# Kernel tuning notes

Measured on AMD Instinct MI355X. Metric: run time of the kernel, lower is better.

Reference implementation:

```python
import jax, jax.numpy as jnp
import numpy as np

K_WRITE = 4
NUM_SLOTS = 16
VOCAB = 50257
D = 512


def layer_norm(x, g, b, eps=1e-5):
    mu = jnp.mean(x, axis=-1, keepdims=True)
    var = jnp.mean((x - mu) ** 2, axis=-1, keepdims=True)
    return (x - mu) * jax.lax.rsqrt(var + eps) * g + b


def setup_inputs() -> dict:
    key = jax.random.key(0)
    ks = jax.random.split(key, 16)
    B, T = 32, 2048
    s = lambda *sh: 1.0 / np.sqrt(sh[0])
    seq = jax.random.randint(ks[0], (B, T), 0, VOCAB)
    embed = jax.random.normal(ks[1], (VOCAB, D), jnp.float32) * 0.02
    W1 = jax.random.normal(ks[2], (D, 2 * D), jnp.float32) * s(D)
    b1 = jnp.zeros((2 * D,), jnp.float32)
    W2 = jax.random.normal(ks[3], (2 * D, D), jnp.float32) * s(2 * D)
    b2 = jnp.zeros((D,), jnp.float32)
    ln_g = jnp.ones((D,), jnp.float32)
    ln_b = jnp.zeros((D,), jnp.float32)
    Wg = jax.random.normal(ks[4], (D, NUM_SLOTS), jnp.float32) * s(D)
    bg = jnp.zeros((NUM_SLOTS,), jnp.float32)
    Wr = jax.random.normal(ks[5], (D, D), jnp.float32) * s(D)
    br = jnp.zeros((D,), jnp.float32)
    Wo = jax.random.normal(ks[6], (D, VOCAB), jnp.float32) * s(D)
    bo = jnp.zeros((VOCAB,), jnp.float32)
    return dict(seq=seq, embed=embed, W1=W1, b1=b1, W2=W2, b2=b2, ln_g=ln_g,
                ln_b=ln_b, Wg=Wg, bg=bg, Wr=Wr, br=br, Wo=Wo, bo=bo)


def forward(seq, embed, W1, b1, W2, b2, ln_g, ln_b, Wg, bg, Wr, br, Wo, bo):
    # Encoder: embed -> FFN residual -> layernorm
    h = embed[seq]                                  # [B,T,D]
    ff = jax.nn.relu(h @ W1 + b1) @ W2 + b2
    hiddens = layer_norm(h + ff, ln_g, ln_b)        # [B,T,D]

    ctx_h = hiddens[:, :-1, :]                      # [B,T-1,D]
    B, Tm1, Dd = ctx_h.shape
    k_w = min(K_WRITE, Tm1)

    # write_to_memory: gate -> topk -> gather -> scatter into zero memory
    gate_scores = jnp.mean(ctx_h @ Wg + bg, axis=-1)          # [B,T-1]
    _, top_idx = jax.lax.top_k(gate_scores, k_w)              # [B,k_w]
    gathered = jnp.take_along_axis(ctx_h, top_idx[:, :, None], axis=1)  # [B,k_w,D]
    slot_idx = jnp.arange(k_w) % NUM_SLOTS                    # unique since k_w<=slots
    mem = jnp.zeros((B, NUM_SLOTS, Dd), ctx_h.dtype).at[:, slot_idx, :].set(gathered)

    # small attention read
    q = hiddens[:, -1, :] @ Wr + br                 # [B,D]
    scores = jnp.einsum('bsd,bd->bs', mem, q)       # [B,slots]
    attn = jax.nn.softmax(scores, axis=-1)
    ctx = jnp.einsum('bs,bsd->bd', attn, mem)       # [B,D]
    return ctx @ Wo + bo                            # [B,vocab]


def reference(seq, embed, W1, b1, W2, b2, ln_g, ln_b, Wg, bg, Wr, br, Wo, bo):
    return forward(seq, embed, W1, b1, W2, b2, ln_g, ln_b, Wg, bg, Wr, br, Wo, bo)
```

## Files before the change

### kernel.cpp

```cpp
#include <hip/hip_runtime.h>
#include <stdint.h>

typedef __attribute__((ext_vector_type(8))) short bf16x8;
typedef __attribute__((ext_vector_type(4))) float f32x4;
typedef __attribute__((ext_vector_type(16))) float f32x16;
typedef unsigned short ushortT;

#define DEV static __device__ __forceinline__

DEV unsigned short f2bf(float x) {
  union { float f; unsigned u; } v; v.f = x;
  unsigned r = v.u + 0x7fffu + ((v.u >> 16) & 1u);
  return (unsigned short)(r >> 16);
}
DEV float bf2f(unsigned short b) {
  union { unsigned u; float f; } v; v.u = ((unsigned)b) << 16; return v.f;
}
DEV void gll16(const void* g, void* l) {
  __builtin_amdgcn_global_load_lds((const __attribute__((address_space(1))) void*)g,
                                   (__attribute__((address_space(3))) void*)l, 16, 0, 0);
}

#define VMW(n) asm volatile("s_waitcnt vmcnt(" #n ")" ::: "memory")
#define RAWBAR() __builtin_amdgcn_s_barrier()
#define SCHED0() __builtin_amdgcn_sched_barrier(0)

__global__ void kPrep(const float* __restrict__ W1, const float* __restrict__ W2,
                      const float* __restrict__ Wg, const float* __restrict__ ln_g,
                      ushortT* __restrict__ W1t, ushortT* __restrict__ W2t,
                      float* __restrict__ gw, float* __restrict__ wgm) {
  const size_t t = (size_t)blockIdx.x * 256 + threadIdx.x;
  if (t < 524288) {
    int n = (int)(t & 1023), k = (int)(t >> 10);
    W1t[(size_t)n * 512 + k] = f2bf(W1[(size_t)k * 1024 + n]);
  } else if (t < 1048576) {
    size_t u = t - 524288;
    int n = (int)(u & 511), k = (int)(u >> 9);
    W2t[(size_t)n * 1024 + k] = f2bf(W2[(size_t)k * 512 + n]);
  } else if (t < 1048576 + 512) {
    int c = (int)(t - 1048576);
    float s = 0.f;
    for (int j = 0; j < 16; ++j) s += Wg[c * 16 + j];
    float m = s * (1.0f / 16.0f);
    wgm[c] = m;
    gw[c] = ln_g[c] * m;
  }
}

__global__ void kPrep2(const float* __restrict__ gw, const float* __restrict__ wgm,
                       const float* __restrict__ ln_b, const float* __restrict__ bg,
                       float* __restrict__ consts) {
  const int tid = threadIdx.x;
  float a = gw[tid];
  float c = ln_b[tid] * wgm[tid];
  #pragma unroll
  for (int s = 1; s < 64; s <<= 1) { a += __shfl_xor(a, s); c += __shfl_xor(c, s); }
  __shared__ float red[8][2];
  const int wv = tid >> 6, ln = tid & 63;
  if (ln == 0) { red[wv][0] = a; red[wv][1] = c; }
  __syncthreads();
  if (tid == 0) {
    float Cg = 0, Cb0 = 0;
    for (int k = 0; k < 8; ++k) { Cg += red[k][0]; Cb0 += red[k][1]; }
    float bgm = 0;
    for (int j = 0; j < 16; ++j) bgm += bg[j];
    bgm *= (1.0f / 16.0f);
    consts[0] = Cg; consts[1] = Cb0 + bgm; consts[2] = bgm;
  }
}

__global__ void kEmbed(const int* __restrict__ seq, const float* __restrict__ embed,
                       ushortT* __restrict__ h) {
  const size_t t = (size_t)blockIdx.x * 256 + threadIdx.x;
  const size_t row = t >> 6;
  const int seg = (int)(t & 63) * 8;
  const int tok = seq[row];
  const float4* src = (const float4*)(embed + (size_t)tok * 512 + seg);
  float4 x = src[0], y = src[1];
  uint4 u;
  u.x = (unsigned)f2bf(x.x) | ((unsigned)f2bf(x.y) << 16);
  u.y = (unsigned)f2bf(x.z) | ((unsigned)f2bf(x.w) << 16);
  u.z = (unsigned)f2bf(y.x) | ((unsigned)f2bf(y.y) << 16);
  u.w = (unsigned)f2bf(y.z) | ((unsigned)f2bf(y.w) << 16);
  *(uint4*)(h + row * 512 + seg) = u;
}

__global__ __launch_bounds__(512, 2) void kG1p(const ushortT* __restrict__ h,
                                               const ushortT* __restrict__ W1t,
                                               const float* __restrict__ b1,
                                               ushortT* __restrict__ Y) {
  __shared__ __align__(16) ushortT SH[32768];
  const int tid = threadIdx.x, w = tid >> 6, l = tid & 63;
  const int b = blockIdx.x, xcd = b & 7, loc = b >> 3;
  const int nt = loc & 3, mtl = loc >> 2;
  const size_t m0 = (size_t)(xcd * 16 + mtl) * 256;
  const int n0 = nt * 256;
  const int rl = l & 15, gq = l >> 4;
  f32x4 acc[4][8] = {};

  auto stage = [&](int buf, int k0) {
    #pragma unroll
    for (int q = 0; q < 2; ++q) {
      const int c = w * 2 + q;
      gll16(h + (m0 + c * 16 + rl) * 512 + k0 + gq * 8, &SH[buf * 8192 + c * 512]);
      gll16(W1t + (size_t)(n0 + c * 16 + rl) * 512 + k0 + gq * 8, &SH[16384 + buf * 8192 + c * 512]);
    }
  };

  const int wr = w >> 1, wc = w & 1, l8 = l * 8;
  auto compute = [&](int buf) {
    bf16x8 a[4], bb[8];
    #pragma unroll
    for (int i = 0; i < 4; ++i)
      a[i] = *(const bf16x8*)&SH[buf * 8192 + (wr * 4 + i) * 512 + l8];
    #pragma unroll
    for (int j = 0; j < 8; ++j)
      bb[j] = *(const bf16x8*)&SH[16384 + buf * 8192 + (wc * 8 + j) * 512 + l8];
    #pragma unroll
    for (int i = 0; i < 4; ++i)
      #pragma unroll
      for (int j = 0; j < 8; ++j)
        acc[i][j] = __builtin_amdgcn_mfma_f32_16x16x32_bf16(a[i], bb[j], acc[i][j], 0, 0, 0);
  };

  stage(0, 0);
  VMW(0); RAWBAR();
  for (int t = 0; t < 16; ++t) {
    if (t < 15) stage((t + 1) & 1, (t + 1) * 32);
    SCHED0();
    compute(t & 1);
    SCHED0();
    VMW(0); RAWBAR();
  }

  float bv[8];
  #pragma unroll
  for (int j = 0; j < 8; ++j) bv[j] = b1[n0 + wc * 128 + j * 16 + rl];

  #pragma unroll
  for (int P = 0; P < 4; ++P) {
    __syncthreads();
    if (wr == P) {
      #pragma unroll
      for (int i = 0; i < 4; ++i) {
        #pragma unroll
        for (int j = 0; j < 8; ++j) {
          const int cl = wc * 128 + j * 16 + rl;
          #pragma unroll
          for (int r = 0; r < 4; ++r) {
            const int lr = i * 16 + gq * 4 + r;
            float v = acc[i][j][r] + bv[j];
            v = v > 0.0f ? v : 0.0f;
            SH[lr * 266 + cl] = f2bf(v);
          }
        }
      }
    }
    __syncthreads();
    #pragma unroll
    for (int it = 0; it < 4; ++it) {
      const int row = it * 16 + (tid >> 5);
      const int c8 = (tid & 31) * 8;
      uint4 v = *(const uint4*)&SH[row * 266 + c8];
      *(uint4*)&Y[(m0 + P * 64 + row) * 1024 + n0 + c8] = v;
    }
  }
}

__global__ __launch_bounds__(512, 2) void kG2p(const ushortT* __restrict__ Yb,
                                               const ushortT* __restrict__ W2t,
                                               const ushortT* __restrict__ h,
                                               const float* __restrict__ b2,
                                               const float* __restrict__ gw,
                                               float* __restrict__ partS, int R0) {
  __shared__ __align__(16) ushortT As[2][256 * 32];
  __shared__ __align__(16) ushortT Bs[2][128 * 32];
  __shared__ float part[256][2][3];
  const int tid = threadIdx.x, w = tid >> 6, l = tid & 63;
  const int b = blockIdx.x, xcd = b & 7, loc = b >> 3;
  const int nt = loc & 3, mtl = loc >> 2;
  const size_t m0 = (size_t)(xcd * 16 + mtl) * 256;
  const int n0 = nt * 128;
  const int rl = l & 15, gq = l >> 4;
  f32x4 acc[4][4] = {};

  auto stage = [&](int buf, int k0) {
    #pragma unroll
    for (int q = 0; q < 2; ++q) {
      const int c = w * 2 + q;
      gll16(Yb + (m0 + c * 16 + rl) * 1024 + k0 + gq * 8, &As[buf][c * 512]);
    }
    gll16(W2t + (size_t)(n0 + w * 16 + rl) * 1024 + k0 + gq * 8, &Bs[buf][w * 512]);
  };

  const int wr = w >> 1, wc = w & 1, l8 = l * 8;
  auto compute = [&](int buf) {
    bf16x8 a[4], bb[4];
    #pragma unroll
    for (int i = 0; i < 4; ++i)
      a[i] = *(const bf16x8*)&As[buf][(wr * 4 + i) * 512 + l8];
    #pragma unroll
    for (int j = 0; j < 4; ++j)
      bb[j] = *(const bf16x8*)&Bs[buf][(wc * 4 + j) * 512 + l8];
    #pragma unroll
    for (int i = 0; i < 4; ++i)
      #pragma unroll
      for (int j = 0; j < 4; ++j)
        acc[i][j] = __builtin_amdgcn_mfma_f32_16x16x32_bf16(a[i], bb[j], acc[i][j], 0, 0, 0);
  };

  stage(0, 0);
  VMW(0); RAWBAR();
  for (int t = 0; t < 32; ++t) {
    if (t < 31) stage((t + 1) & 1, (t + 1) * 32);
    SCHED0();
    compute(t & 1);
    SCHED0();
    VMW(0); RAWBAR();
  }

  #pragma unroll
  for (int i = 0; i < 4; ++i) {
    #pragma unroll
    for (int r = 0; r < 4; ++r) {
      const int rowl = wr * 64 + i * 16 + gq * 4 + r;
      const size_t grow = (size_t)R0 + m0 + rowl;
      float s1 = 0, s2 = 0, s3 = 0;
      #pragma unroll
      for (int j = 0; j < 4; ++j) {
        const int col = n0 + wc * 64 + j * 16 + rl;
        const float z = acc[i][j][r] + b2[col] + bf2f(h[grow * 512 + col]);
        s1 += z; s2 += z * z; s3 += z * gw[col];
      }
      #pragma unroll
      for (int s = 1; s < 16; s <<= 1) {
        s1 += __shfl_xor(s1, s);
        s2 += __shfl_xor(s2, s);
        s3 += __shfl_xor(s3, s);
      }
      if (rl == 0) { part[rowl][wc][0] = s1; part[rowl][wc][1] = s2; part[rowl][wc][2] = s3; }
    }
  }
  __syncthreads();
  if (tid < 256) {
    const size_t grow = (size_t)R0 + m0 + tid;
    const float S1 = part[tid][0][0] + part[tid][1][0];
    const float S2 = part[tid][0][1] + part[tid][1][1];
    const float S3 = part[tid][0][2] + part[tid][1][2];
    float* p = partS + grow * 16 + nt * 4;
    p[0] = S1; p[1] = S2; p[2] = S3;
  }
}

__global__ void kTop(const float* __restrict__ partS, const float* __restrict__ consts,
                     float* __restrict__ scores, int* __restrict__ cidx,
                     int* __restrict__ ccnt) {
  const int b = blockIdx.x, tid = threadIdx.x;
  const float Cg = consts[0], Cb = consts[1];
  float v0 = -1e30f, v1 = -1e30f, v2 = -1e30f, v3 = -1e30f;
  for (int i = tid; i < 2047; i += 256) {
    const size_t row = (size_t)b * 2048 + i;
    const float* p = partS + row * 16;
    const float S1 = p[0] + p[4] + p[8] + p[12];
    const float S2 = p[1] + p[5] + p[9] + p[13];
    const float S3 = p[2] + p[6] + p[10] + p[14];
    const float mu = S1 * (1.0f / 512.0f);
    const float var = S2 * (1.0f / 512.0f) - mu * mu;
    const float x = rsqrtf(var + 1e-5f) * (S3 - mu * Cg) + Cb;
    scores[row] = x;
    if (x > v3) {
      if (x > v0)      { v3 = v2; v2 = v1; v1 = v0; v0 = x; }
      else if (x > v1) { v3 = v2; v2 = v1; v1 = x; }
      else if (x > v2) { v3 = v2; v2 = x; }
      else             { v3 = x; }
    }
  }
  __shared__ float lv[256][4];
  lv[tid][0] = v0; lv[tid][1] = v1; lv[tid][2] = v2; lv[tid][3] = v3;
  __syncthreads();
  for (int s = 128; s > 0; s >>= 1) {
    if (tid < s) {
      float m[8] = { lv[tid][0], lv[tid][1], lv[tid][2], lv[tid][3],
                     lv[tid + s][0], lv[tid + s][1], lv[tid + s][2], lv[tid + s][3] };
      #pragma unroll
      for (int k = 0; k < 4; ++k) {
        int mx = k;
        #pragma unroll
        for (int j2 = k + 1; j2 < 8; ++j2) if (m[j2] > m[mx]) mx = j2;
        const float tv = m[k]; m[k] = m[mx]; m[mx] = tv;
        lv[tid][k] = m[k];
      }
    }
    __syncthreads();
  }
  __shared__ int cnt;
  __shared__ float thr;
  if (tid == 0) { thr = lv[0][3] - 0.03f; cnt = 0; }
  __syncthreads();
  const float th = thr;
  const float* sc = scores + (size_t)b * 2048;
  for (int i = tid; i < 2047; i += 256) {
    if (sc[i] >= th) {
      const int p = atomicAdd(&cnt, 1);
      if (p < 24) cidx[b * 24 + p] = i;
    }
  }
  __syncthreads();
  if (tid == 0) ccnt[b] = cnt < 24 ? cnt : 24;
}

__global__ void kCompact(const int* __restrict__ ccnt, const int* __restrict__ cidx,
                         int* __restrict__ offs, int* __restrict__ rowsb,
                         int* __restrict__ rowsl, int* __restrict__ plast,
                         int* __restrict__ nrp) {
  const int tid = threadIdx.x;
  if (tid >= 32) return;
  int off = 0, nc = 0;
  for (int k = 0; k < 32; ++k) { const int c = ccnt[k]; if (k < tid) off += c; nc += c; }
  offs[tid] = off;
  const int cnt = ccnt[tid];
  for (int j = 0; j < cnt; ++j) { rowsb[off + j] = tid; rowsl[off + j] = cidx[tid * 24 + j]; }
  rowsb[nc + tid] = tid; rowsl[nc + tid] = 2047; plast[tid] = nc + tid;
  if (tid == 0) { offs[32] = nc; nrp[0] = nc + 32; }
}

__global__ void kGather(const int* __restrict__ nrp, const int* __restrict__ rowsb,
                        const int* __restrict__ rowsl, const int* __restrict__ seq,
                        const float* __restrict__ embed, float* __restrict__ H2) {
  const int p = blockIdx.x;
  if (p >= nrp[0]) return;
  const int b = rowsb[p], lr = rowsl[p];
  const size_t gr = (size_t)b * 2048 + lr;
  const int tok = seq[gr];
  const float* src = embed + (size_t)tok * 512;
  float* dst = H2 + (size_t)p * 512;
  for (int c = threadIdx.x; c < 512; c += 128) dst[c] = src[c];
}

__global__ __launch_bounds__(256) void kR1(const int* __restrict__ nrp,
                                           const float* __restrict__ H2,
                                           const float* __restrict__ W1,
                                           const float* __restrict__ b1,
                                           float* __restrict__ Y2) {
  const int p = blockIdx.y;
  if (p >= nrp[0]) return;
  const int col = blockIdx.x * 256 + threadIdx.x;
  __shared__ float hrow[512];
  for (int c = threadIdx.x; c < 512; c += 256) hrow[c] = H2[(size_t)p * 512 + c];
  __syncthreads();
  float a0 = 0, a1 = 0, a2 = 0, a3 = 0;
  #pragma unroll 4
  for (int k = 0; k < 512; k += 4) {
    a0 = fmaf(hrow[k + 0], W1[(size_t)(k + 0) * 1024 + col], a0);
    a1 = fmaf(hrow[k + 1], W1[(size_t)(k + 1) * 1024 + col], a1);
    a2 = fmaf(hrow[k + 2], W1[(size_t)(k + 2) * 1024 + col], a2);
    a3 = fmaf(hrow[k + 3], W1[(size_t)(k + 3) * 1024 + col], a3);
  }
  const float v = a0 + a1 + a2 + a3 + b1[col];
  Y2[(size_t)p * 1024 + col] = v > 0.0f ? v : 0.0f;
}

__global__ __launch_bounds__(256) void kR2(const int* __restrict__ nrp,
                                           const float* __restrict__ Y2,
                                           const float* __restrict__ W2,
                                           const float* __restrict__ b2,
                                           float* __restrict__ F2) {
  const int p = blockIdx.y;
  if (p >= nrp[0]) return;
  const int col = blockIdx.x * 256 + threadIdx.x;
  __shared__ float yrow[1024];
  for (int c = threadIdx.x; c < 1024; c += 256) yrow[c] = Y2[(size_t)p * 1024 + c];
  __syncthreads();
  float a0 = 0, a1 = 0, a2 = 0, a3 = 0;
  #pragma unroll 4
  for (int k = 0; k < 1024; k += 4) {
    a0 = fmaf(yrow[k + 0], W2[(size_t)(k + 0) * 512 + col], a0);
    a1 = fmaf(yrow[k + 1], W2[(size_t)(k + 1) * 512 + col], a1);
    a2 = fmaf(yrow[k + 2], W2[(size_t)(k + 2) * 512 + col], a2);
    a3 = fmaf(yrow[k + 3], W2[(size_t)(k + 3) * 512 + col], a3);
  }
  F2[(size_t)p * 512 + col] = a0 + a1 + a2 + a3 + b2[col];
}

__global__ void kR3(const int* __restrict__ nrp, const float* __restrict__ H2,
                    const float* __restrict__ F2, const float* __restrict__ ln_g,
                    const float* __restrict__ ln_b, const float* __restrict__ wgm,
                    const float* __restrict__ consts, float* __restrict__ LNR,
                    float* __restrict__ cscore) {
  const int p = blockIdx.x;
  if (p >= nrp[0]) return;
  const int tid = threadIdx.x;
  const int c0 = tid, c1 = tid + 256;
  const float z0 = H2[(size_t)p * 512 + c0] + F2[(size_t)p * 512 + c0];
  const float z1 = H2[(size_t)p * 512 + c1] + F2[(size_t)p * 512 + c1];
  float s1 = z0 + z1, s2 = z0 * z0 + z1 * z1;
  #pragma unroll
  for (int s = 1; s < 64; s <<= 1) { s1 += __shfl_xor(s1, s); s2 += __shfl_xor(s2, s); }
  __shared__ float red[4][2];
  __shared__ float stats[2];
  const int wv = tid >> 6, ln = tid & 63;
  if (ln == 0) { red[wv][0] = s1; red[wv][1] = s2; }
  __syncthreads();
  if (tid == 0) {
    const float S1 = red[0][0] + red[1][0] + red[2][0] + red[3][0];
    const float S2 = red[0][1] + red[1][1] + red[2][1] + red[3][1];
    const float mu = S1 * (1.0f / 512.0f);
    const float var = S2 * (1.0f / 512.0f) - mu * mu;
    stats[0] = mu; stats[1] = rsqrtf(var + 1e-5f);
  }
  __syncthreads();
  const float mu = stats[0], rstd = stats[1];
  const float l0 = (z0 - mu) * rstd * ln_g[c0] + ln_b[c0];
  const float l1 = (z1 - mu) * rstd * ln_g[c1] + ln_b[c1];
  LNR[(size_t)p * 512 + c0] = l0;
  LNR[(size_t)p * 512 + c1] = l1;
  float sp = l0 * wgm[c0] + l1 * wgm[c1];
  #pragma unroll
  for (int s = 1; s < 64; s <<= 1) sp += __shfl_xor(sp, s);
  if (ln == 0) red[wv][0] = sp;
  __syncthreads();
  if (tid == 0) cscore[p] = red[0][0] + red[1][0] + red[2][0] + red[3][0] + consts[2];
}

__global__ void kSel(const int* __restrict__ ccnt, const int* __restrict__ offs,
                     const int* __restrict__ rowsl, const int* __restrict__ plast,
                     const float* __restrict__ cscore, const float* __restrict__ LNR,
                     const float* __restrict__ Wr, const float* __restrict__ br,
                     float* __restrict__ ctx, ushortT* __restrict__ ctxB) {
  const int b = blockIdx.x, tid = threadIdx.x;
  __shared__ int psel[4];
  __shared__ float lnl[512];
  __shared__ float qs[512];
  __shared__ float aw[4];
  __shared__ float red[4][4];
  if (tid == 0) {
    const int cnt = ccnt[b], off = offs[b];
    float scv[24]; int lr[24]; bool tk[24];
    for (int j = 0; j < cnt; ++j) { scv[j] = cscore[off + j]; lr[j] = rowsl[off + j]; tk[j] = false; }
    for (int k = 0; k < 4; ++k) {
      int best = -1;
      for (int j = 0; j < cnt; ++j) {
        if (tk[j]) continue;
        if (best < 0 || scv[j] > scv[best] || (scv[j] == scv[best] && lr[j] < lr[best])) best = j;
      }
      tk[best] = true;
      psel[k] = off + best;
    }
  }
  __syncthreads();
  const int pl = plast[b];
  for (int c = tid; c < 512; c += 256) lnl[c] = LNR[(size_t)pl * 512 + c];
  __syncthreads();
  #pragma unroll
  for (int cc = 0; cc < 2; ++cc) {
    const int col = tid + cc * 256;
    float s = br[col];
    for (int d = 0; d < 512; ++d) s = fmaf(lnl[d], Wr[(size_t)d * 512 + col], s);
    qs[col] = s;
  }
  __syncthreads();
  const int p0 = psel[0], p1 = psel[1], p2 = psel[2], p3 = psel[3];
  float ps[4] = {0, 0, 0, 0};
  for (int d = tid; d < 512; d += 256) {
    const float qv = qs[d];
    ps[0] = fmaf(qv, LNR[(size_t)p0 * 512 + d], ps[0]);
    ps[1] = fmaf(qv, LNR[(size_t)p1 * 512 + d], ps[1]);
    ps[2] = fmaf(qv, LNR[(size_t)p2 * 512 + d], ps[2]);
    ps[3] = fmaf(qv, LNR[(size_t)p3 * 512 + d], ps[3]);
  }
  #pragma unroll
  for (int s = 1; s < 64; s <<= 1) {
    ps[0] += __shfl_xor(ps[0], s); ps[1] += __shfl_xor(ps[1], s);
    ps[2] += __shfl_xor(ps[2], s); ps[3] += __shfl_xor(ps[3], s);
  }
  const int wv = tid >> 6, ln = tid & 63;
  if (ln == 0) { red[wv][0] = ps[0]; red[wv][1] = ps[1]; red[wv][2] = ps[2]; red[wv][3] = ps[3]; }
  __syncthreads();
  if (tid == 0) {
    const float s0 = red[0][0] + red[1][0] + red[2][0] + red[3][0];
    const float s1 = red[0][1] + red[1][1] + red[2][1] + red[3][1];
    const float s2 = red[0][2] + red[1][2] + red[2][2] + red[3][2];
    const float s3 = red[0][3] + red[1][3] + red[2][3] + red[3][3];
    const float m = fmaxf(fmaxf(fmaxf(s0, s1), fmaxf(s2, s3)), 0.0f);
    const float e0 = expf(s0 - m), e1 = expf(s1 - m), e2 = expf(s2 - m), e3 = expf(s3 - m);
    const float den = e0 + e1 + e2 + e3 + 12.0f * expf(-m);
    aw[0] = e0 / den; aw[1] = e1 / den; aw[2] = e2 / den; aw[3] = e3 / den;
  }
  __syncthreads();
  const float a0 = aw[0], a1 = aw[1], a2 = aw[2], a3 = aw[3];
  #pragma unroll
  for (int cc = 0; cc < 2; ++cc) {
    const int col = tid + cc * 256;
    const float v = a0 * LNR[(size_t)p0 * 512 + col] + a1 * LNR[(size_t)p1 * 512 + col]
                  + a2 * LNR[(size_t)p2 * 512 + col] + a3 * LNR[(size_t)p3 * 512 + col];
    ctx[(size_t)b * 512 + col] = v;
    ctxB[(size_t)b * 512 + col] = f2bf(v);
  }
}

__global__ __launch_bounds__(512) void kOutM(const ushortT* __restrict__ ctxB,
                                             const float* __restrict__ Wo,
                                             float* __restrict__ partial) {
  const int tid = threadIdx.x, w = tid >> 6, l = tid & 63;
  const int ky = blockIdx.y;
  int col = blockIdx.x * 256 + w * 32 + (l & 31);
  const bool cv = col < 50257;
  if (!cv) col = 50256;
  const int kg = (l >> 5) * 8;
  const int kb = ky * 256;
  bf16x8 afr[16];
  #pragma unroll
  for (int ks = 0; ks < 16; ++ks)
    afr[ks] = *(const bf16x8*)&ctxB[(size_t)(l & 31) * 512 + kb + ks * 16 + kg];
  f32x16 acc = {};
  #pragma unroll
  for (int ks = 0; ks < 16; ++ks) {
    const float* wp = Wo + (size_t)(kb + ks * 16 + kg) * 50257 + col;
    float wv[8];
    #pragma unroll
    for (int j = 0; j < 8; ++j) wv[j] = wp[(size_t)j * 50257];
    bf16x8 bfr;
    #pragma unroll
    for (int j = 0; j < 8; ++j) bfr[j] = (short)f2bf(wv[j]);
    acc = __builtin_amdgcn_mfma_f32_32x32x16_bf16(afr[ks], bfr, acc, 0, 0, 0);
  }
  if (cv) {
    #pragma unroll
    for (int r = 0; r < 16; ++r) {
      const int row = (r & 3) + 8 * (r >> 2) + 4 * (l >> 5);
      partial[((size_t)ky * 32 + row) * 50257 + col] = acc[r];
    }
  }
}

__global__ __launch_bounds__(256) void kOutRed(const float* __restrict__ partial,
                                               const float* __restrict__ bo,
                                               float* __restrict__ out) {
  const size_t i = (size_t)blockIdx.x * 256 + threadIdx.x;
  if (i >= (size_t)32 * 50257) return;
  const int col = (int)(i % 50257);
  float s = bo[col];
  #pragma unroll
  for (int q = 0; q < 2; ++q) s += partial[(size_t)q * 32 * 50257 + i];
  out[i] = s;
}

extern "C" void kernel_launch(void* const* d_in, const int* in_sizes, int n_in,
                              void* d_out, int out_size, void* d_ws, size_t ws_size,
                              hipStream_t stream) {
  const int*   seq   = (const int*)  d_in[0];
  const float* embed = (const float*)d_in[1];
  const float* W1    = (const float*)d_in[2];
  const float* b1    = (const float*)d_in[3];
  const float* W2    = (const float*)d_in[4];
  const float* b2    = (const float*)d_in[5];
  const float* ln_g  = (const float*)d_in[6];
  const float* ln_b  = (const float*)d_in[7];
  const float* Wg    = (const float*)d_in[8];
  const float* bg    = (const float*)d_in[9];
  const float* Wr    = (const float*)d_in[10];
  const float* br    = (const float*)d_in[11];
  const float* Wo    = (const float*)d_in[12];
  const float* bo    = (const float*)d_in[13];
  float* out = (float*)d_out;
  char* ws = (char*)d_ws;

  ushortT* W1t   = (ushortT*)(ws + 0);
  ushortT* W2t   = (ushortT*)(ws + 1048576);
  float* gw      = (float*)(ws + 2097152);
  float* wgm     = (float*)(ws + 2099200);
  float* consts  = (float*)(ws + 2101248);
  ushortT* h     = (ushortT*)(ws + 2101504);
  ushortT* Ybuf  = (ushortT*)(ws + 69210368);
  float* partial = (float*)(ws + 69210368);
  float* scores  = (float*)(ws + 136319232);
  int* cidx      = (int*)(ws + 136581376);
  int* ccnt      = (int*)(ws + 136584448);
  int* offs      = (int*)(ws + 136584576);
  int* nrp       = (int*)(ws + 136584832);
  int* plast     = (int*)(ws + 136585088);
  int* rowsb     = (int*)(ws + 136585344);
  int* rowsl     = (int*)(ws + 136588672);
  float* partS   = (float*)(ws + 136592000);
  float* H2      = (float*)(ws + 136592000);
  float* Y2      = (float*)(ws + 138295936);
  float* F2      = (float*)(ws + 141703808);
  float* LNR     = (float*)(ws + 143407744);
  float* csc     = (float*)(ws + 145111680);
  float* ctxb    = (float*)(ws + 145115008);
  ushortT* ctxB  = (ushortT*)(ws + 145180544);

  kPrep <<<4098, 256, 0, stream>>>(W1, W2, Wg, ln_g, W1t, W2t, gw, wgm);
  kPrep2<<<1, 512, 0, stream>>>(gw, wgm, ln_b, bg, consts);
  kEmbed<<<16384, 256, 0, stream>>>(seq, embed, h);
  for (int c = 0; c < 2; ++c) {
    kG1p<<<512, 512, 0, stream>>>(h + (size_t)c * 32768 * 512, W1t, b1, Ybuf);
    kG2p<<<512, 512, 0, stream>>>(Ybuf, W2t, h, b2, gw, partS, c * 32768);
  }
  kTop    <<<32, 256, 0, stream>>>(partS, consts, scores, cidx, ccnt);
  kCompact<<<1, 64, 0, stream>>>(ccnt, cidx, offs, rowsb, rowsl, plast, nrp);
  kGather <<<800, 128, 0, stream>>>(nrp, rowsb, rowsl, seq, embed, H2);
  kR1<<<dim3(4, 800), 256, 0, stream>>>(nrp, H2, W1, b1, Y2);
  kR2<<<dim3(2, 800), 256, 0, stream>>>(nrp, Y2, W2, b2, F2);
  kR3<<<800, 256, 0, stream>>>(nrp, H2, F2, ln_g, ln_b, wgm, consts, LNR, csc);
  kSel<<<32, 256, 0, stream>>>(ccnt, offs, rowsl, plast, csc, LNR, Wr, br, ctxb, ctxB);
  kOutM<<<dim3(197, 2), 512, 0, stream>>>(ctxB, Wo, partial);
  kOutRed<<<(32 * 50257 + 255) / 256, 256, 0, stream>>>(partial, bo, out);
}
```

Baseline: 447.7 us.

## Double K-tile depth in FFN GEMMs and raise wave priority around MFMA

Both FFN GEMM kernels now stage 64-wide K tiles per iteration (as two 32-wide halves) instead of 32-wide ones. This halves the number of main-loop iterations and barriers. The wait on the next prefetch moves to before compute using a partial vmcnt, and MFMA bursts are bracketed with s_setprio to favour waves issuing matrix math. The trade-off is a larger LDS footprint (128 KB in the first GEMM, about 100 KB in the second), which likely limits each CU to one block despite launch bounds requesting two, reducing latency hiding across blocks.

```diff
diff --git a/kernel.cpp b/kernel.cpp
--- a/kernel.cpp
+++ b/kernel.cpp
@@ -24,6 +24,8 @@
 #define VMW(n) asm volatile("s_waitcnt vmcnt(" #n ")" ::: "memory")
 #define RAWBAR() __builtin_amdgcn_s_barrier()
 #define SCHED0() __builtin_amdgcn_sched_barrier(0)
+#define PRIO1() __builtin_amdgcn_s_setprio(1)
+#define PRIO0() __builtin_amdgcn_s_setprio(0)
 
 __global__ void kPrep(const float* __restrict__ W1, const float* __restrict__ W2,
                       const float* __restrict__ Wg, const float* __restrict__ ln_g,
@@ -89,7 +91,7 @@
                                                const ushortT* __restrict__ W1t,
                                                const float* __restrict__ b1,
                                                ushortT* __restrict__ Y) {
-  __shared__ __align__(16) ushortT SH[32768];
+  __shared__ __align__(16) ushortT SH[65536];
   const int tid = threadIdx.x, w = tid >> 6, l = tid & 63;
   const int b = blockIdx.x, xcd = b & 7, loc = b >> 3;
   const int nt = loc & 3, mtl = loc >> 2;
@@ -100,37 +102,55 @@
 
   auto stage = [&](int buf, int k0) {
     #pragma unroll
-    for (int q = 0; q < 2; ++q) {
-      const int c = w * 2 + q;
-      gll16(h + (m0 + c * 16 + rl) * 512 + k0 + gq * 8, &SH[buf * 8192 + c * 512]);
-      gll16(W1t + (size_t)(n0 + c * 16 + rl) * 512 + k0 + gq * 8, &SH[16384 + buf * 8192 + c * 512]);
+    for (int kh = 0; kh < 2; ++kh) {
+      #pragma unroll
+      for (int q = 0; q < 2; ++q) {
+        const int c = w * 2 + q;
+        gll16(h + (m0 + c * 16 + rl) * 512 + k0 + kh * 32 + gq * 8,
+              &SH[buf * 16384 + kh * 8192 + c * 512]);
+        gll16(W1t + (size_t)(n0 + c * 16 + rl) * 512 + k0 + kh * 32 + gq * 8,
+              &SH[32768 + buf * 16384 + kh * 8192 + c * 512]);
+      }
     }
   };
 
   const int wr = w >> 1, wc = w & 1, l8 = l * 8;
-  auto compute = [&](int buf) {
-    bf16x8 a[4], bb[8];
-    #pragma unroll
-    for (int i = 0; i < 4; ++i)
-      a[i] = *(const bf16x8*)&SH[buf * 8192 + (wr * 4 + i) * 512 + l8];
-    #pragma unroll
-    for (int j = 0; j < 8; ++j)
-      bb[j] = *(const bf16x8*)&SH[16384 + buf * 8192 + (wc * 8 + j) * 512 + l8];
-    #pragma unroll
-    for (int i = 0; i < 4; ++i)
-      #pragma unroll
-      for (int j = 0; j < 8; ++j)
-        acc[i][j] = __builtin_amdgcn_mfma_f32_16x16x32_bf16(a[i], bb[j], acc[i][j], 0, 0, 0);
+  auto tile_compute = [&](int buf) {
+    #pragma unroll
+    for (int q = 0; q < 4; ++q) {
+      const int kh = q >> 1, nh = q & 1;
+      bf16x8 a[4], bb[4];
+      #pragma unroll
+      for (int i = 0; i < 4; ++i)
+        a[i] = *(const bf16x8*)&SH[buf * 16384 + kh * 8192 + (wr * 4 + i) * 512 + l8];
+      #pragma unroll
+      for (int jj = 0; jj < 4; ++jj)
+        bb[jj] = *(const bf16x8*)&SH[32768 + buf * 16384 + kh * 8192 + (wc * 8 + nh * 4 + jj) * 512 + l8];
+      SCHED0();
+      PRIO1();
+      #pragma unroll
+      for (int i = 0; i < 4; ++i)
+        #pragma unroll
+        for (int jj = 0; jj < 4; ++jj)
+          acc[i][nh * 4 + jj] = __builtin_amdgcn_mfma_f32_16x16x32_bf16(a[i], bb[jj], acc[i][nh * 4 + jj], 0, 0, 0);
+      PRIO0();
+    }
   };
 
   stage(0, 0);
   VMW(0); RAWBAR();
-  for (int t = 0; t < 16; ++t) {
-    if (t < 15) stage((t + 1) & 1, (t + 1) * 32);
-    SCHED0();
-    compute(t & 1);
-    SCHED0();
-    VMW(0); RAWBAR();
+  int buf = 0;
+  for (int t = 0; t < 8; ++t) {
+    if (t < 7) {
+      stage(buf ^ 1, (t + 1) * 64);
+      VMW(8);
+    } else {
+      VMW(0);
+    }
+    RAWBAR();
+    tile_compute(buf);
+    RAWBAR();
+    buf ^= 1;
   }
 
   float bv[8];
@@ -173,8 +193,7 @@
                                                const float* __restrict__ b2,
                                                const float* __restrict__ gw,
                                                float* __restrict__ partS, int R0) {
-  __shared__ __align__(16) ushortT As[2][256 * 32];
-  __shared__ __align__(16) ushortT Bs[2][128 * 32];
+  __shared__ __align__(16) ushortT SH[49152];
   __shared__ float part[256][2][3];
   const int tid = threadIdx.x, w = tid >> 6, l = tid & 63;
   const int b = blockIdx.x, xcd = b & 7, loc = b >> 3;
@@ -186,37 +205,54 @@
 
   auto stage = [&](int buf, int k0) {
     #pragma unroll
-    for (int q = 0; q < 2; ++q) {
-      const int c = w * 2 + q;
-      gll16(Yb + (m0 + c * 16 + rl) * 1024 + k0 + gq * 8, &As[buf][c * 512]);
-    }
-    gll16(W2t + (size_t)(n0 + w * 16 + rl) * 1024 + k0 + gq * 8, &Bs[buf][w * 512]);
+    for (int kh = 0; kh < 2; ++kh) {
+      #pragma unroll
+      for (int q = 0; q < 2; ++q) {
+        const int c = w * 2 + q;
+        gll16(Yb + (m0 + c * 16 + rl) * 1024 + k0 + kh * 32 + gq * 8,
+              &SH[buf * 16384 + kh * 8192 + c * 512]);
+      }
+      gll16(W2t + (size_t)(n0 + w * 16 + rl) * 1024 + k0 + kh * 32 + gq * 8,
+            &SH[32768 + buf * 8192 + kh * 4096 + w * 512]);
+    }
   };
 
   const int wr = w >> 1, wc = w & 1, l8 = l * 8;
-  auto compute = [&](int buf) {
-    bf16x8 a[4], bb[4];
-    #pragma unroll
-    for (int i = 0; i < 4; ++i)
-      a[i] = *(const bf16x8*)&As[buf][(wr * 4 + i) * 512 + l8];
-    #pragma unroll
-    for (int j = 0; j < 4; ++j)
-      bb[j] = *(const bf16x8*)&Bs[buf][(wc * 4 + j) * 512 + l8];
-    #pragma unroll
-    for (int i = 0; i < 4; ++i)
-      #pragma unroll
-      for (int j = 0; j < 4; ++j)
-        acc[i][j] = __builtin_amdgcn_mfma_f32_16x16x32_bf16(a[i], bb[j], acc[i][j], 0, 0, 0);
+  auto tile_compute = [&](int buf) {
+    #pragma unroll
+    for (int kh = 0; kh < 2; ++kh) {
+      bf16x8 a[4], bb[4];
+      #pragma unroll
+      for (int i = 0; i < 4; ++i)
+        a[i] = *(const bf16x8*)&SH[buf * 16384 + kh * 8192 + (wr * 4 + i) * 512 + l8];
+      #pragma unroll
+      for (int jj = 0; jj < 4; ++jj)
+        bb[jj] = *(const bf16x8*)&SH[32768 + buf * 8192 + kh * 4096 + (wc * 4 + jj) * 512 + l8];
+      SCHED0();
+      PRIO1();
+      #pragma unroll
+      for (int i = 0; i < 4; ++i)
+        #pragma unroll
+        for (int jj = 0; jj < 4; ++jj)
+          acc[i][jj] = __builtin_amdgcn_mfma_f32_16x16x32_bf16(a[i], bb[jj], acc[i][jj], 0, 0, 0);
+      PRIO0();
+    }
   };
 
   stage(0, 0);
   VMW(0); RAWBAR();
-  for (int t = 0; t < 32; ++t) {
-    if (t < 31) stage((t + 1) & 1, (t + 1) * 32);
-    SCHED0();
-    compute(t & 1);
-    SCHED0();
-    VMW(0); RAWBAR();
+  int buf = 0;
+  for (int t = 0; t < 16; ++t) {
+    if (t < 15) {
+      stage(buf ^ 1, (t + 1) * 64);
+      VMW(6);
+    } else {
+      VMW(0);
+    }
+    RAWBAR();
+    tile_compute(buf);
+    RAWBAR();
+    buf ^= 1;
   }
 
   #pragma unroll
```

Measured after the change: 505.4 us. 12.9% more time.

## Triple-buffer GEMM K-loops, halve G1 N-tile, split output GEMM K four ways

Applied to the files above, without the earlier changes.

Both FFN GEMM kernels switch from double buffering with a full vmcnt(0) wait per step to a three-stage global_load_lds pipeline with partial vmcnt waits. The goal is to keep two tiles of loads in flight while MFMAs run. kG1p also narrows its N tile from 256 to 128 and doubles the grid to 1024 blocks, which lowers accumulator register pressure. kOutM splits K into four slices instead of two to get more parallel blocks streaming Wo, at the cost of a larger partial buffer and extra reads in the reduction kernel.

```diff
diff --git a/kernel.cpp b/kernel.cpp
--- a/kernel.cpp
+++ b/kernel.cpp
@@ -89,53 +89,52 @@
                                                const ushortT* __restrict__ W1t,
                                                const float* __restrict__ b1,
                                                ushortT* __restrict__ Y) {
-  __shared__ __align__(16) ushortT SH[32768];
+  __shared__ __align__(16) ushortT SH[36864];
   const int tid = threadIdx.x, w = tid >> 6, l = tid & 63;
   const int b = blockIdx.x, xcd = b & 7, loc = b >> 3;
-  const int nt = loc & 3, mtl = loc >> 2;
+  const int nt = loc & 7, mtl = loc >> 3;
   const size_t m0 = (size_t)(xcd * 16 + mtl) * 256;
-  const int n0 = nt * 256;
+  const int n0 = nt * 128;
   const int rl = l & 15, gq = l >> 4;
-  f32x4 acc[4][8] = {};
+  f32x4 acc[4][4] = {};
 
   auto stage = [&](int buf, int k0) {
     #pragma unroll
     for (int q = 0; q < 2; ++q) {
       const int c = w * 2 + q;
       gll16(h + (m0 + c * 16 + rl) * 512 + k0 + gq * 8, &SH[buf * 8192 + c * 512]);
-      gll16(W1t + (size_t)(n0 + c * 16 + rl) * 512 + k0 + gq * 8, &SH[16384 + buf * 8192 + c * 512]);
-    }
+    }
+    gll16(W1t + (size_t)(n0 + w * 16 + rl) * 512 + k0 + gq * 8, &SH[24576 + buf * 4096 + w * 512]);
   };
 
   const int wr = w >> 1, wc = w & 1, l8 = l * 8;
   auto compute = [&](int buf) {
-    bf16x8 a[4], bb[8];
+    bf16x8 a[4], bb[4];
     #pragma unroll
     for (int i = 0; i < 4; ++i)
       a[i] = *(const bf16x8*)&SH[buf * 8192 + (wr * 4 + i) * 512 + l8];
     #pragma unroll
-    for (int j = 0; j < 8; ++j)
-      bb[j] = *(const bf16x8*)&SH[16384 + buf * 8192 + (wc * 8 + j) * 512 + l8];
+    for (int j = 0; j < 4; ++j)
+      bb[j] = *(const bf16x8*)&SH[24576 + buf * 4096 + (wc * 4 + j) * 512 + l8];
     #pragma unroll
     for (int i = 0; i < 4; ++i)
       #pragma unroll
-      for (int j = 0; j < 8; ++j)
+      for (int j = 0; j < 4; ++j)
         acc[i][j] = __builtin_amdgcn_mfma_f32_16x16x32_bf16(a[i], bb[j], acc[i][j], 0, 0, 0);
   };
 
-  stage(0, 0);
-  VMW(0); RAWBAR();
+  stage(0, 0); stage(1, 32); stage(2, 64);
   for (int t = 0; t < 16; ++t) {
-    if (t < 15) stage((t + 1) & 1, (t + 1) * 32);
-    SCHED0();
-    compute(t & 1);
-    SCHED0();
-    VMW(0); RAWBAR();
-  }
-
-  float bv[8];
-  #pragma unroll
-  for (int j = 0; j < 8; ++j) bv[j] = b1[n0 + wc * 128 + j * 16 + rl];
+    if (t <= 13) { VMW(6); } else if (t == 14) { VMW(3); } else { VMW(0); }
+    RAWBAR(); SCHED0();
+    compute(t % 3);
+    SCHED0(); RAWBAR();
+    if (t <= 12) stage(t % 3, (t + 3) * 32);
+  }
+
+  float bv[4];
+  #pragma unroll
+  for (int j = 0; j < 4; ++j) bv[j] = b1[n0 + wc * 64 + j * 16 + rl];
 
   #pragma unroll
   for (int P = 0; P < 4; ++P) {
@@ -144,24 +143,24 @@
       #pragma unroll
       for (int i = 0; i < 4; ++i) {
         #pragma unroll
-        for (int j = 0; j < 8; ++j) {
-          const int cl = wc * 128 + j * 16 + rl;
+        for (int j = 0; j < 4; ++j) {
+          const int cl = wc * 64 + j * 16 + rl;
           #pragma unroll
           for (int r = 0; r < 4; ++r) {
             const int lr = i * 16 + gq * 4 + r;
             float v = acc[i][j][r] + bv[j];
             v = v > 0.0f ? v : 0.0f;
-            SH[lr * 266 + cl] = f2bf(v);
+            SH[lr * 136 + cl] = f2bf(v);
           }
         }
       }
     }
     __syncthreads();
     #pragma unroll
-    for (int it = 0; it < 4; ++it) {
-      const int row = it * 16 + (tid >> 5);
-      const int c8 = (tid & 31) * 8;
-      uint4 v = *(const uint4*)&SH[row * 266 + c8];
+    for (int it = 0; it < 2; ++it) {
+      const int row = it * 32 + (tid >> 4);
+      const int c8 = (tid & 15) * 8;
+      uint4 v = *(const uint4*)&SH[row * 136 + c8];
       *(uint4*)&Y[(m0 + P * 64 + row) * 1024 + n0 + c8] = v;
     }
   }
@@ -173,8 +172,7 @@
                                                const float* __restrict__ b2,
                                                const float* __restrict__ gw,
                                                float* __restrict__ partS, int R0) {
-  __shared__ __align__(16) ushortT As[2][256 * 32];
-  __shared__ __align__(16) ushortT Bs[2][128 * 32];
+  __shared__ __align__(16) ushortT SH[36864];
   __shared__ float part[256][2][3];
   const int tid = threadIdx.x, w = tid >> 6, l = tid & 63;
   const int b = blockIdx.x, xcd = b & 7, loc = b >> 3;
@@ -188,9 +186,9 @@
     #pragma unroll
     for (int q = 0; q < 2; ++q) {
       const int c = w * 2 + q;
-      gll16(Yb + (m0 + c * 16 + rl) * 1024 + k0 + gq * 8, &As[buf][c * 512]);
-    }
-    gll16(W2t + (size_t)(n0 + w * 16 + rl) * 1024 + k0 + gq * 8, &Bs[buf][w * 512]);
+      gll16(Yb + (m0 + c * 16 + rl) * 1024 + k0 + gq * 8, &SH[buf * 8192 + c * 512]);
+    }
+    gll16(W2t + (size_t)(n0 + w * 16 + rl) * 1024 + k0 + gq * 8, &SH[24576 + buf * 4096 + w * 512]);
   };
 
   const int wr = w >> 1, wc = w & 1, l8 = l * 8;
@@ -198,10 +196,10 @@
     bf16x8 a[4], bb[4];
     #pragma unroll
     for (int i = 0; i < 4; ++i)
-      a[i] = *(const bf16x8*)&As[buf][(wr * 4 + i) * 512 + l8];
+      a[i] = *(const bf16x8*)&SH[buf * 8192 + (wr * 4 + i) * 512 + l8];
     #pragma unroll
     for (int j = 0; j < 4; ++j)
-      bb[j] = *(const bf16x8*)&Bs[buf][(wc * 4 + j) * 512 + l8];
+      bb[j] = *(const bf16x8*)&SH[24576 + buf * 4096 + (wc * 4 + j) * 512 + l8];
     #pragma unroll
     for (int i = 0; i < 4; ++i)
       #pragma unroll
@@ -209,14 +207,13 @@
         acc[i][j] = __builtin_amdgcn_mfma_f32_16x16x32_bf16(a[i], bb[j], acc[i][j], 0, 0, 0);
   };
 
-  stage(0, 0);
-  VMW(0); RAWBAR();
+  stage(0, 0); stage(1, 32); stage(2, 64);
   for (int t = 0; t < 32; ++t) {
-    if (t < 31) stage((t + 1) & 1, (t + 1) * 32);
-    SCHED0();
-    compute(t & 1);
-    SCHED0();
-    VMW(0); RAWBAR();
+    if (t <= 29) { VMW(6); } else if (t == 30) { VMW(3); } else { VMW(0); }
+    RAWBAR(); SCHED0();
+    compute(t % 3);
+    SCHED0(); RAWBAR();
+    if (t <= 28) stage(t % 3, (t + 3) * 32);
   }
 
   #pragma unroll
@@ -507,14 +504,14 @@
   const bool cv = col < 50257;
   if (!cv) col = 50256;
   const int kg = (l >> 5) * 8;
-  const int kb = ky * 256;
-  bf16x8 afr[16];
-  #pragma unroll
-  for (int ks = 0; ks < 16; ++ks)
+  const int kb = ky * 128;
+  bf16x8 afr[8];
+  #pragma unroll
+  for (int ks = 0; ks < 8; ++ks)
     afr[ks] = *(const bf16x8*)&ctxB[(size_t)(l & 31) * 512 + kb + ks * 16 + kg];
   f32x16 acc = {};
   #pragma unroll
-  for (int ks = 0; ks < 16; ++ks) {
+  for (int ks = 0; ks < 8; ++ks) {
     const float* wp = Wo + (size_t)(kb + ks * 16 + kg) * 50257 + col;
     float wv[8];
     #pragma unroll
@@ -541,7 +538,7 @@
   const int col = (int)(i % 50257);
   float s = bo[col];
   #pragma unroll
-  for (int q = 0; q < 2; ++q) s += partial[(size_t)q * 32 * 50257 + i];
+  for (int q = 0; q < 4; ++q) s += partial[(size_t)q * 32 * 50257 + i];
   out[i] = s;
 }
 
@@ -594,7 +591,7 @@
   kPrep2<<<1, 512, 0, stream>>>(gw, wgm, ln_b, bg, consts);
   kEmbed<<<16384, 256, 0, stream>>>(seq, embed, h);
   for (int c = 0; c < 2; ++c) {
-    kG1p<<<512, 512, 0, stream>>>(h + (size_t)c * 32768 * 512, W1t, b1, Ybuf);
+    kG1p<<<1024, 512, 0, stream>>>(h + (size_t)c * 32768 * 512, W1t, b1, Ybuf);
     kG2p<<<512, 512, 0, stream>>>(Ybuf, W2t, h, b2, gw, partS, c * 32768);
   }
   kTop    <<<32, 256, 0, stream>>>(partS, consts, scores, cidx, ccnt);
@@ -604,6 +601,6 @@
   kR2<<<dim3(2, 800), 256, 0, stream>>>(nrp, Y2, W2, b2, F2);
   kR3<<<800, 256, 0, stream>>>(nrp, H2, F2, ln_g, ln_b, wgm, consts, LNR, csc);
   kSel<<<32, 256, 0, stream>>>(ccnt, offs, rowsl, plast, csc, LNR, Wr, br, ctxb, ctxB);
-  kOutM<<<dim3(197, 2), 512, 0, stream>>>(ctxB, Wo, partial);
+  kOutM<<<dim3(197, 4), 512, 0, stream>>>(ctxB, Wo, partial);
   kOutRed<<<(32 * 50257 + 255) / 256, 256, 0, stream>>>(partial, bo, out);
 }
```

New measurement: 438.9 us. About the same (-2.0%).
